# Kernel tuning notes

Hardware: AMD Instinct MI355X
Metric: run time of the kernel (lower is better)

## Reference

```python
import jax, jax.numpy as jnp
import numpy as np

N, B, F, H = 100000, 128, 512, 256


def setup_inputs() -> dict:
    key = jax.random.key(0)
    ks = jax.random.split(key, 9)
    pos = jax.random.normal(ks[0], (N, 3), dtype=jnp.float32)
    mass_center = jax.random.normal(ks[1], (B, 3), dtype=jnp.float32)
    scaler = jax.random.normal(ks[2], (N, F), dtype=jnp.float32)
    vector = jax.random.normal(ks[3], (N, 3), dtype=jnp.float32)
    batch_index = jax.random.randint(ks[4], (N,), 0, B, dtype=jnp.int64)
    # MLP params (Linear(F,H) -> act -> Linear(H,1)), kaiming-uniform-ish init
    lim1 = 1.0 / np.sqrt(F)
    lim2 = 1.0 / np.sqrt(H)
    W1 = jax.random.uniform(ks[5], (F, H), minval=-lim1, maxval=lim1, dtype=jnp.float32)
    b1 = jax.random.uniform(ks[6], (H,), minval=-lim1, maxval=lim1, dtype=jnp.float32)
    W2 = jax.random.uniform(ks[7], (H, 1), minval=-lim2, maxval=lim2, dtype=jnp.float32)
    b2 = jax.random.uniform(ks[8], (1,), minval=-lim2, maxval=lim2, dtype=jnp.float32)
    return {"pos": pos, "mass_center": mass_center, "scaler": scaler,
            "vector": vector, "batch_index": batch_index,
            "W1": W1, "b1": b1, "W2": W2, "b2": b2}


def reference(pos, mass_center, scaler, vector, batch_index, W1, b1, W2, b2):
    # gather per-graph mass center to nodes: [N,3]
    mass_center_vec = pos - mass_center[batch_index]
    # tiny 2-layer MLP on node scalars: [N,F] -> [N,H] -> [N,1]
    h = jax.nn.silu(scaler @ W1 + b1)
    q_i = h @ W2 + b2                         # [N,1]
    # squared L2 norm of displacement: [N,1]
    r2_i = jnp.sum(mass_center_vec * mass_center_vec, axis=1, keepdims=True)
    # scatter-sum per graph: [B,1]
    out = jax.ops.segment_sum(q_i * r2_i, batch_index, num_segments=B)
    return out
```

## Files before the change

kernel.cpp:

```cpp
#include <hip/hip_runtime.h>
#include <hip/hip_bf16.h>
#include <stdint.h>

#define F_DIM 512
#define H_DIM 256
#define B_DIM 128
#define M_BLK 64
#define NCHUNK 16
#define NBUF 3

typedef __bf16 bf16x8 __attribute__((ext_vector_type(8)));
typedef float  f32x4  __attribute__((ext_vector_type(4)));

__global__ __launch_bounds__(256) void convert_w1_kernel(
    const float* __restrict__ W1, __bf16* __restrict__ W1t) {
    int t = blockIdx.x * 256 + threadIdx.x;
    int c = t >> 9;
    int k = t & 511;
    W1t[t] = (__bf16)W1[k * H_DIM + c];
}

__device__ inline void gload_lds16(const float* g, float* lds) {
    __builtin_amdgcn_global_load_lds(
        (const __attribute__((address_space(1))) uint32_t*)g,
        (__attribute__((address_space(3))) uint32_t*)lds, 16, 0, 0);
}
__device__ inline void gload_lds16b(const __bf16* g, __bf16* lds) {
    __builtin_amdgcn_global_load_lds(
        (const __attribute__((address_space(1))) uint32_t*)g,
        (__attribute__((address_space(3))) uint32_t*)lds, 16, 0, 0);
}

template<bool USE_PARTIAL>
__global__ __launch_bounds__(512) void fused_mlp_kernel(
    const float* __restrict__ pos,
    const float* __restrict__ mass_center,
    const float* __restrict__ scaler,
    const int*   __restrict__ batch_index,
    const __bf16* __restrict__ W1t,
    const float* __restrict__ b1,
    const float* __restrict__ W2,
    const float* __restrict__ b2,
    float* __restrict__ outp,
    int N)
{
    __shared__ float  A_lds[NBUF][M_BLK][32];
    __shared__ __bf16 Bc_lds[NBUF][H_DIM][32];
    __shared__ float  q_lds[M_BLK];
    __shared__ float  pb[B_DIM];

    const int tid    = threadIdx.x;
    const int lane   = tid & 63;
    const int wid    = tid >> 6;
    const int wave_m = wid >> 2;
    const int wave_n = wid & 3;
    const int lrow   = lane & 15;
    const int kq     = (lane >> 4) * 8;
    const int row_base = blockIdx.x * M_BLK;

    if (tid < M_BLK) q_lds[tid] = 0.f;
    if (USE_PARTIAL && tid < B_DIM) pb[tid] = 0.f;
    __syncthreads();

    const int srow = tid >> 3;
    const int sseg = (tid & 7) ^ (srow & 7);
    int grA = row_base + srow; if (grA >= N) grA = N - 1;
    const float* gsA = scaler + (size_t)grA * F_DIM + sseg * 4;

    const int s0   = tid;
    const int s1   = 512 + tid;
    const __bf16* gsB0 = W1t + (size_t)(s0 >> 2) * F_DIM + (s0 & 3) * 8;
    const __bf16* gsB1 = W1t + (size_t)(s1 >> 2) * F_DIM + (s1 & 3) * 8;

#define STAGE(buf, c) do {                                                    \
        gload_lds16 (gsA  + (c) * 32, &A_lds[(buf)][0][0] + wid * 256);       \
        gload_lds16b(gsB0 + (c) * 32, &Bc_lds[(buf)][0][0] + wid * 512);      \
        gload_lds16b(gsB1 + (c) * 32, &Bc_lds[(buf)][0][0] + 4096 + wid * 512); \
    } while (0)

    f32x4 acc[2][4];
    #pragma unroll
    for (int mi = 0; mi < 2; ++mi)
        #pragma unroll
        for (int ni = 0; ni < 4; ++ni)
            acc[mi][ni] = (f32x4){0.f, 0.f, 0.f, 0.f};

    STAGE(0, 0);
    STAGE(1, 1);

    #pragma unroll
    for (int kc = 0; kc < NCHUNK; ++kc) {
        if (kc + 2 < NCHUNK)
            STAGE((kc + 2) % NBUF, kc + 2);

        if (kc < NCHUNK - 2)       asm volatile("s_waitcnt vmcnt(6)" ::: "memory");
        else if (kc == NCHUNK - 2) asm volatile("s_waitcnt vmcnt(3)" ::: "memory");
        else                       asm volatile("s_waitcnt vmcnt(0)" ::: "memory");
        __builtin_amdgcn_s_barrier();

        const int buf = kc % NBUF;
        bf16x8 af[2];
        #pragma unroll
        for (int mi = 0; mi < 2; ++mi) {
            const int rA = wave_m * 32 + mi * 16 + lrow;
            const int sw = (rA & 7) << 4;
            const char* rb = (const char*)&A_lds[buf][0][0] + rA * 128;
            f32x4 a0 = *(const f32x4*)(rb + ((kq * 4) ^ sw));
            f32x4 a1 = *(const f32x4*)(rb + ((kq * 4 + 16) ^ sw));
            #pragma unroll
            for (int j = 0; j < 4; ++j) {
                af[mi][j]     = (__bf16)a0[j];
                af[mi][4 + j] = (__bf16)a1[j];
            }
        }
        bf16x8 bfrag[4];
        #pragma unroll
        for (int ni = 0; ni < 4; ++ni) {
            const int col = wave_n * 64 + ni * 16 + lrow;
            bfrag[ni] = *(const bf16x8*)(&Bc_lds[buf][col][0] + kq);
        }
        #pragma unroll
        for (int mi = 0; mi < 2; ++mi)
            #pragma unroll
            for (int ni = 0; ni < 4; ++ni)
                acc[mi][ni] = __builtin_amdgcn_mfma_f32_16x16x32_bf16(
                    af[mi], bfrag[ni], acc[mi][ni], 0, 0, 0);

        __builtin_amdgcn_s_barrier();
    }
#undef STAGE

    float qp[2][4];
    #pragma unroll
    for (int mi = 0; mi < 2; ++mi)
        #pragma unroll
        for (int r = 0; r < 4; ++r) qp[mi][r] = 0.f;

    #pragma unroll
    for (int ni = 0; ni < 4; ++ni) {
        int c = wave_n * 64 + ni * 16 + lrow;
        float b1c = b1[c];
        float w2c = W2[c];
        #pragma unroll
        for (int mi = 0; mi < 2; ++mi)
            #pragma unroll
            for (int r = 0; r < 4; ++r) {
                float h = acc[mi][ni][r] + b1c;
                float s = h / (1.0f + __expf(-h));
                qp[mi][r] += s * w2c;
            }
    }
    #pragma unroll
    for (int off = 1; off < 16; off <<= 1)
        #pragma unroll
        for (int mi = 0; mi < 2; ++mi)
            #pragma unroll
            for (int r = 0; r < 4; ++r)
                qp[mi][r] += __shfl_xor(qp[mi][r], off, 64);

    if ((lane & 15) == 0) {
        int rgrp = lane >> 4;
        #pragma unroll
        for (int mi = 0; mi < 2; ++mi)
            #pragma unroll
            for (int r = 0; r < 4; ++r)
                atomicAdd(&q_lds[wave_m * 32 + mi * 16 + rgrp * 4 + r], qp[mi][r]);
    }
    __syncthreads();

    if (tid < M_BLK) {
        int grow = row_base + tid;
        if (grow < N) {
            float q  = q_lds[tid] + b2[0];
            int   bi = batch_index[grow];
            float dx = pos[grow * 3 + 0] - mass_center[bi * 3 + 0];
            float dy = pos[grow * 3 + 1] - mass_center[bi * 3 + 1];
            float dz = pos[grow * 3 + 2] - mass_center[bi * 3 + 2];
            float val = q * (dx * dx + dy * dy + dz * dz);
            if (USE_PARTIAL) atomicAdd(&pb[bi], val);
            else             atomicAdd(&outp[bi], val);
        }
    }
    if (USE_PARTIAL) {
        __syncthreads();
        if (tid < B_DIM)
            outp[(size_t)blockIdx.x * B_DIM + tid] = pb[tid];
    }
}

__global__ __launch_bounds__(256) void reduce_partials_kernel(
    const float* __restrict__ partial, float* __restrict__ out, int nblk) {
    int b = blockIdx.x;
    float s = 0.f;
    for (int i = threadIdx.x; i < nblk; i += 256)
        s += partial[(size_t)i * B_DIM + b];
    #pragma unroll
    for (int off = 1; off < 64; off <<= 1)
        s += __shfl_xor(s, off, 64);
    __shared__ float wsum[4];
    if ((threadIdx.x & 63) == 0) wsum[threadIdx.x >> 6] = s;
    __syncthreads();
    if (threadIdx.x == 0)
        out[b] = wsum[0] + wsum[1] + wsum[2] + wsum[3];
}

extern "C" void kernel_launch(void* const* d_in, const int* in_sizes, int n_in,
                              void* d_out, int out_size, void* d_ws, size_t ws_size,
                              hipStream_t stream) {
    const float* pos         = (const float*)d_in[0];
    const float* mass_center = (const float*)d_in[1];
    const float* scaler      = (const float*)d_in[2];
    const int*   batch_index = (const int*)d_in[4];
    const float* W1          = (const float*)d_in[5];
    const float* b1          = (const float*)d_in[6];
    const float* W2          = (const float*)d_in[7];
    const float* b2          = (const float*)d_in[8];
    float* out = (float*)d_out;
    (void)n_in; (void)out_size;

    int N = in_sizes[0] / 3;
    int nblk = (N + M_BLK - 1) / M_BLK;

    size_t w1t_bytes  = (size_t)F_DIM * H_DIM * sizeof(__bf16);
    size_t part_bytes = (size_t)nblk * B_DIM * sizeof(float);

    __bf16* W1t = (__bf16*)d_ws;
    convert_w1_kernel<<<(F_DIM * H_DIM) / 256, 256, 0, stream>>>(W1, W1t);

    if (ws_size >= w1t_bytes + part_bytes) {
        float* partial = (float*)((char*)d_ws + w1t_bytes);
        fused_mlp_kernel<true><<<nblk, 512, 0, stream>>>(
            pos, mass_center, scaler, batch_index, W1t, b1, W2, b2, partial, N);
        reduce_partials_kernel<<<B_DIM, 256, 0, stream>>>(partial, out, nblk);
    } else {
        hipMemsetAsync(out, 0, B_DIM * sizeof(float), stream);
        fused_mlp_kernel<false><<<nblk, 512, 0, stream>>>(
            pos, mass_center, scaler, batch_index, W1t, b1, W2, b2, out, N);
    }
}
```

Before: 85.24 us.

## Halve K-chunk LDS staging and restructure pipeline to raise block occupancy

```diff
diff --git a/kernel.cpp b/kernel.cpp
--- a/kernel.cpp
+++ b/kernel.cpp
@@ -6,8 +6,8 @@
 #define H_DIM 256
 #define B_DIM 128
 #define M_BLK 64
-#define NCHUNK 16
-#define NBUF 3
+#define NHALF 32
+#define HBUF 3
 
 typedef __bf16 bf16x8 __attribute__((ext_vector_type(8)));
 typedef float  f32x4  __attribute__((ext_vector_type(4)));
@@ -32,7 +32,7 @@
 }
 
 template<bool USE_PARTIAL>
-__global__ __launch_bounds__(512) void fused_mlp_kernel(
+__global__ __launch_bounds__(512, 8) void fused_mlp_kernel(
     const float* __restrict__ pos,
     const float* __restrict__ mass_center,
     const float* __restrict__ scaler,
@@ -44,8 +44,8 @@
     float* __restrict__ outp,
     int N)
 {
-    __shared__ float  A_lds[NBUF][M_BLK][32];
-    __shared__ __bf16 Bc_lds[NBUF][H_DIM][32];
+    __shared__ float  A_lds[HBUF][M_BLK][16];
+    __shared__ __bf16 B_lds[HBUF][H_DIM][16];
     __shared__ float  q_lds[M_BLK];
     __shared__ float  pb[B_DIM];
 
@@ -60,22 +60,20 @@
 
     if (tid < M_BLK) q_lds[tid] = 0.f;
     if (USE_PARTIAL && tid < B_DIM) pb[tid] = 0.f;
-    __syncthreads();
-
-    const int srow = tid >> 3;
-    const int sseg = (tid & 7) ^ (srow & 7);
-    int grA = row_base + srow; if (grA >= N) grA = N - 1;
-    const float* gsA = scaler + (size_t)grA * F_DIM + sseg * 4;
-
-    const int s0   = tid;
-    const int s1   = 512 + tid;
-    const __bf16* gsB0 = W1t + (size_t)(s0 >> 2) * F_DIM + (s0 & 3) * 8;
-    const __bf16* gsB1 = W1t + (size_t)(s1 >> 2) * F_DIM + (s1 & 3) * 8;
-
-#define STAGE(buf, c) do {                                                    \
-        gload_lds16 (gsA  + (c) * 32, &A_lds[(buf)][0][0] + wid * 256);       \
-        gload_lds16b(gsB0 + (c) * 32, &Bc_lds[(buf)][0][0] + wid * 512);      \
-        gload_lds16b(gsB1 + (c) * 32, &Bc_lds[(buf)][0][0] + 4096 + wid * 512); \
+
+    const int arow = tid >> 2;
+    const int aseg = (tid & 3) ^ (arow & 3);
+    int grA = row_base + arow; if (grA >= N) grA = N - 1;
+    const float* gsA = scaler + (size_t)grA * F_DIM + aseg * 4;
+
+    const int bcol = tid >> 1;
+    const int bks  = (tid & 1) ^ ((bcol >> 2) & 1);
+    const __bf16* gsB = W1t + (size_t)bcol * F_DIM + bks * 8;
+
+#define STAGE(buf, h) do {                                                    \
+        if (wid < 4)                                                          \
+            gload_lds16(gsA + (h) * 16, &A_lds[(buf)][0][0] + wid * 256);     \
+        gload_lds16b(gsB + (h) * 16, &B_lds[(buf)][0][0] + wid * 512);        \
     } while (0)
 
     f32x4 acc[2][4];
@@ -87,26 +85,30 @@
 
     STAGE(0, 0);
     STAGE(1, 1);
-
-    #pragma unroll
-    for (int kc = 0; kc < NCHUNK; ++kc) {
-        if (kc + 2 < NCHUNK)
-            STAGE((kc + 2) % NBUF, kc + 2);
-
-        if (kc < NCHUNK - 2)       asm volatile("s_waitcnt vmcnt(6)" ::: "memory");
-        else if (kc == NCHUNK - 2) asm volatile("s_waitcnt vmcnt(3)" ::: "memory");
-        else                       asm volatile("s_waitcnt vmcnt(0)" ::: "memory");
+    STAGE(2, 2);
+
+    #pragma unroll
+    for (int t = 0; t < NHALF / 2; ++t) {
+        if (t < NHALF / 2 - 1) {
+            if (wid < 4) asm volatile("s_waitcnt vmcnt(2)" ::: "memory");
+            else         asm volatile("s_waitcnt vmcnt(1)" ::: "memory");
+        } else {
+            asm volatile("s_waitcnt vmcnt(0)" ::: "memory");
+        }
         __builtin_amdgcn_s_barrier();
 
-        const int buf = kc % NBUF;
+        const int b0 = (2 * t) % HBUF;
+        const int b1 = (2 * t + 1) % HBUF;
+        const int bsel = (kq & 16) ? b1 : b0;
+        const int offs = (kq & 8) >> 2;
+
         bf16x8 af[2];
         #pragma unroll
         for (int mi = 0; mi < 2; ++mi) {
             const int rA = wave_m * 32 + mi * 16 + lrow;
-            const int sw = (rA & 7) << 4;
-            const char* rb = (const char*)&A_lds[buf][0][0] + rA * 128;
-            f32x4 a0 = *(const f32x4*)(rb + ((kq * 4) ^ sw));
-            f32x4 a1 = *(const f32x4*)(rb + ((kq * 4 + 16) ^ sw));
+            const float* rbase = &A_lds[0][0][0] + bsel * 1024 + rA * 16;
+            f32x4 a0 = *(const f32x4*)(rbase + ((offs    ) ^ (rA & 3)) * 4);
+            f32x4 a1 = *(const f32x4*)(rbase + ((offs + 1) ^ (rA & 3)) * 4);
             #pragma unroll
             for (int j = 0; j < 4; ++j) {
                 af[mi][j]     = (__bf16)a0[j];
@@ -117,7 +119,9 @@
         #pragma unroll
         for (int ni = 0; ni < 4; ++ni) {
             const int col = wave_n * 64 + ni * 16 + lrow;
-            bfrag[ni] = *(const bf16x8*)(&Bc_lds[buf][col][0] + kq);
+            const int ks  = ((kq & 8) >> 3) ^ ((col >> 2) & 1);
+            bfrag[ni] = *(const bf16x8*)(&B_lds[0][0][0] + bsel * 4096
+                                         + col * 16 + ks * 8);
         }
         #pragma unroll
         for (int mi = 0; mi < 2; ++mi)
@@ -127,6 +131,8 @@
                     af[mi], bfrag[ni], acc[mi][ni], 0, 0, 0);
 
         __builtin_amdgcn_s_barrier();
+        if (2 * t + 3 < NHALF) STAGE((2 * t + 3) % HBUF, 2 * t + 3);
+        if (2 * t + 4 < NHALF) STAGE((2 * t + 4) % HBUF, 2 * t + 4);
     }
 #undef STAGE
 
```

Result: slower. 149.5 us (+75.4%).
